# Kernel optimization log

Measured on AMD Instinct MI355X. Metric: run time of the kernel, lower is better.

## Reference

```python
import jax, jax.numpy as jnp
import numpy as np

B, T, F, C0, C1, H = 32, 1000, 32, 16, 8, 64
LSNR_SCALE, LSNR_OFFSET = 50.0, -15.0  # lsnr_max=35, lsnr_min=-15


def _conv1x3(x, w, b):
    # x: [N, Cin, T, F]; kernel (1,3), freq padding 1 (stride 1, k=1 so no time context)
    y = jax.lax.conv_general_dilated(x, w, (1, 1), [(0, 0), (1, 1)],
                                     dimension_numbers=('NCHW', 'OIHW', 'NCHW'))
    return y + b[None, :, None, None]


def _ln(x, g, b, eps=1e-5):
    # LayerNorm over the last (freq) axis, as nn.LayerNorm(n_freqs)
    mu = x.mean(-1, keepdims=True)
    var = x.var(-1, keepdims=True)
    return (x - mu) / jnp.sqrt(var + eps) * g + b


def _gru(x, wih, whh, bih, bhh):
    # PyTorch-style GRU. x: [S, N, D] -> (ys [S, N, Hh], h_last [N, Hh])
    Hh = whh.shape[1]
    h0 = jnp.zeros((x.shape[1], Hh), x.dtype)
    def step(h, xt):
        gi = xt @ wih.T + bih
        gh = h @ whh.T + bhh
        ir, iz, inn = jnp.split(gi, 3, axis=-1)
        hr, hz, hn = jnp.split(gh, 3, axis=-1)
        r = jax.nn.sigmoid(ir + hr)
        z = jax.nn.sigmoid(iz + hz)
        n = jnp.tanh(inn + r * hn)
        hnew = (1.0 - z) * n + z * h
        return hnew, hnew
    hT, ys = jax.lax.scan(step, h0, x)
    return ys, hT


def setup_inputs() -> dict:
    key = jax.random.key(0)
    ks = iter(jax.random.split(key, 40))
    def nrm(shape, s=0.02):
        return jax.random.normal(next(ks), shape, jnp.float32) * s
    return {
        'input': jax.random.normal(next(ks), (B, 1, T, F), jnp.float32),
        'conv0_w': nrm((C0, 1, 1, 3)), 'conv0_b': jnp.zeros((C0,), jnp.float32),
        'ln0_g': jnp.ones((F,), jnp.float32), 'ln0_b': jnp.zeros((F,), jnp.float32),
        'conv1_w': nrm((C1, C0, 1, 3)), 'conv1_b': jnp.zeros((C1,), jnp.float32),
        'ln1_g': jnp.ones((F,), jnp.float32), 'ln1_b': jnp.zeros((F,), jnp.float32),
        'q_w': nrm((H, C1, 1, 3)), 'q_b': jnp.zeros((H,), jnp.float32),
        'k_w': nrm((H, C1, 1, 3)), 'k_b': jnp.zeros((H,), jnp.float32),
        'v_w': nrm((H, C1, 1, 3)), 'v_b': jnp.zeros((H,), jnp.float32),
        'gruo_wih': nrm((3 * C1 * F, H * F)), 'gruo_whh': nrm((3 * C1 * F, C1 * F)),
        'gruo_bih': jnp.zeros((3 * C1 * F,), jnp.float32), 'gruo_bhh': jnp.zeros((3 * C1 * F,), jnp.float32),
        'ln_g': jnp.ones((F,), jnp.float32), 'ln_b': jnp.zeros((F,), jnp.float32),
        'grus_wih': nrm((48, C1 * F)), 'grus_whh': nrm((48, 16)),
        'grus_bih': jnp.zeros((48,), jnp.float32), 'grus_bhh': jnp.zeros((48,), jnp.float32),
        'fc_w': nrm((1, 16)), 'fc_b': jnp.zeros((1,), jnp.float32),
        'conv2_w': nrm((1, C1, 1, 3)), 'conv2_b': jnp.zeros((1,), jnp.float32),
        'ln2_g': jnp.ones((F,), jnp.float32), 'ln2_b': jnp.zeros((F,), jnp.float32),
    }


def reference(input, conv0_w, conv0_b, ln0_g, ln0_b, conv1_w, conv1_b, ln1_g, ln1_b,
              q_w, q_b, k_w, k_b, v_w, v_b, gruo_wih, gruo_whh, gruo_bih, gruo_bhh,
              ln_g, ln_b, grus_wih, grus_whh, grus_bih, grus_bhh, fc_w, fc_b,
              conv2_w, conv2_b, ln2_g, ln2_b):
    # conv0/conv1: conv -> LayerNorm(F) -> ReLU
    x0 = jax.nn.relu(_ln(_conv1x3(input, conv0_w, conv0_b), ln0_g, ln0_b))
    x1 = jax.nn.relu(_ln(_conv1x3(x0, conv1_w, conv1_b), ln1_g, ln1_b))  # [B,C1,T,F]
    # SpectalRecurrentAttention (no norm/act on q/k/v convs)
    q = _conv1x3(x1, q_w, q_b).transpose(0, 2, 3, 1)  # [B,T,F,H]
    k = _conv1x3(x1, k_w, k_b).transpose(0, 2, 1, 3)  # [B,T,H,F]
    v = _conv1x3(x1, v_w, v_b).transpose(0, 2, 3, 1)  # [B,T,F,H]
    w = jnp.einsum('btfh,bthg->btfg', q, k) / jnp.sqrt(jnp.float32(H))  # [B,T,F,F]
    # softmax2d: joint softmax over last two (freq x freq) dims
    w = jax.nn.softmax(w.reshape(B, T, F * F), axis=-1).reshape(B, T, F, F)
    att = jnp.einsum('btfg,btgh->btfh', w, v)  # [B,T,F,H]
    gi = att.reshape(B, T, F * H)
    ys, hT = _gru(gi.transpose(1, 0, 2), gruo_wih, gruo_whh, gruo_bih, gruo_bhh)  # over T (batch_first)
    o = ys.transpose(1, 0, 2)  # [B,T,C1*F]
    h_atten = hT[None]  # [1,B,C1*F]
    e = o.reshape(B, T, C1, F).transpose(0, 2, 1, 3)  # [B,C1,T,F]
    # gru_snr is NOT batch_first: it scans over dim0 (= B) of e.transpose(1,2).flatten(2,3) == o
    snr_ys, snr_hT = _gru(o, grus_wih, grus_whh, grus_bih, grus_bhh)  # ys [B,T,16], hT [T,16]
    h_snr = snr_hT[None]  # [1,T,16]
    lsnr = jax.nn.sigmoid(snr_ys @ fc_w.T + fc_b) * LSNR_SCALE + LSNR_OFFSET  # [B,T,1]
    xe = _ln(x1 + e, ln_g, ln_b)
    m = jax.nn.sigmoid(_ln(_conv1x3(xe, conv2_w, conv2_b), ln2_g, ln2_b))  # [B,1,T,F]
    return m, lsnr, h_atten, h_snr
```

## Files before the change

kernel.cpp:

```cpp
#include <hip/hip_runtime.h>


typedef unsigned short u16;
typedef u16 u16x8 __attribute__((ext_vector_type(8)));
typedef short s16x8 __attribute__((ext_vector_type(8)));
typedef float f32x4 __attribute__((ext_vector_type(4)));
typedef _Float16 h2t __attribute__((ext_vector_type(2)));
typedef unsigned int u32x16 __attribute__((ext_vector_type(16)));

__device__ __forceinline__ float sigf(float x) { return 1.f / (1.f + __expf(-x)); }
__device__ __forceinline__ float tanhfast(float x) { return 2.f / (1.f + __expf(-2.f * x)) - 1.f; }
__device__ __forceinline__ float bf2f(u16 s) { union { unsigned u; float f; } x; x.u = ((unsigned)s) << 16; return x.f; }
__device__ __forceinline__ u16 f2bf(float f) {
  union { float f; unsigned u; } x; x.f = f;
  unsigned r = x.u + 0x7fffu + ((x.u >> 16) & 1u);
  return (u16)(r >> 16);
}
__device__ __forceinline__ h2t pk(float a, float b) {
  auto v = __builtin_amdgcn_cvt_pkrtz(a, b);
  union { decltype(v) i; h2t o; } u; u.i = v; return u.o;
}
__device__ __forceinline__ h2t bch(unsigned x) { return __builtin_bit_cast(h2t, x); }

__global__ __launch_bounds__(256) void k_wcvt_all(
    const float* __restrict__ W, u16* __restrict__ Wb,
    const float* __restrict__ Wh, unsigned* __restrict__ Wp)
{
  if (blockIdx.x < 768) {
    const size_t i = ((size_t)blockIdx.x * 256 + threadIdx.x) * 8;
    float4 a = *(const float4*)(W + i);
    float4 b = *(const float4*)(W + i + 4);
    u16x8 o;
    o[0] = f2bf(a.x); o[1] = f2bf(a.y); o[2] = f2bf(a.z); o[3] = f2bf(a.w);
    o[4] = f2bf(b.x); o[5] = f2bf(b.y); o[6] = f2bf(b.z); o[7] = f2bf(b.w);
    *(u16x8*)(Wb + i) = o;
  } else {
    const size_t i = (size_t)(blockIdx.x - 768) * 256 + threadIdx.x;
    float2 a = *(const float2*)(Wh + i * 2);
    Wp[i] = __builtin_bit_cast(unsigned, pk(a.x, a.y));
  }
}

__global__ __launch_bounds__(256) void k_frontend(
    const float* __restrict__ in,
    const float* __restrict__ w0c, const float* __restrict__ b0c,
    const float* __restrict__ g0, const float* __restrict__ be0,
    const float* __restrict__ w1c, const float* __restrict__ b1c,
    const float* __restrict__ g1, const float* __restrict__ be1,
    const float* __restrict__ qw, const float* __restrict__ qb,
    const float* __restrict__ kw, const float* __restrict__ kb,
    const float* __restrict__ vw, const float* __restrict__ vb,
    int bt0, u16* __restrict__ x1g, u16* __restrict__ gi)
{
  const int bt = bt0 + blockIdx.x, tid = threadIdx.x;
  __shared__ float s_in[34];
  __shared__ float s_x0[16][34];
  __shared__ float s_x1[8][34];
  __shared__ float s_q[64][36];
  __shared__ float s_k[64][36];
  __shared__ float s_v[32][68];
  __shared__ float s_sc[32][36];
  __shared__ float s_red[8];
  __shared__ float s_mu[16], s_rs[16];

  if (tid < 32) s_in[1 + tid] = in[(size_t)bt * 32 + tid];
  if (tid == 0) { s_in[0] = 0.f; s_in[33] = 0.f; }
  __syncthreads();

  #pragma unroll
  for (int i = 0; i < 2; ++i) {
    int o = tid + i * 256, c = o >> 5, f = o & 31;
    float a = b0c[c] + w0c[c*3]*s_in[f] + w0c[c*3+1]*s_in[f+1] + w0c[c*3+2]*s_in[f+2];
    s_x0[c][1 + f] = a;
  }
  __syncthreads();
  {
    int c = tid >> 4, i = tid & 15;
    float a = s_x0[c][1 + i], b = s_x0[c][17 + i];
    float s = a + b, ss = a * a + b * b;
    #pragma unroll
    for (int m = 8; m >= 1; m >>= 1) { s += __shfl_xor(s, m); ss += __shfl_xor(ss, m); }
    if (i == 0) { float mu = s * (1.f/32.f); s_mu[c] = mu; s_rs[c] = rsqrtf(ss * (1.f/32.f) - mu*mu + 1e-5f); }
  }
  __syncthreads();
  #pragma unroll
  for (int i = 0; i < 2; ++i) {
    int o = tid + i * 256, c = o >> 5, f = o & 31;
    float v = (s_x0[c][1 + f] - s_mu[c]) * s_rs[c] * g0[f] + be0[f];
    s_x0[c][1 + f] = fmaxf(v, 0.f);
  }
  if (tid < 16) { s_x0[tid][0] = 0.f; s_x0[tid][33] = 0.f; }
  __syncthreads();

  {
    int c = tid >> 5, f = tid & 31;
    float a = b1c[c];
    #pragma unroll
    for (int cc = 0; cc < 16; ++cc) {
      const float* wr = w1c + (c * 16 + cc) * 3;
      a += wr[0]*s_x0[cc][f] + wr[1]*s_x0[cc][f+1] + wr[2]*s_x0[cc][f+2];
    }
    float s = a, ss = a * a;
    #pragma unroll
    for (int m = 16; m >= 1; m >>= 1) { s += __shfl_xor(s, m); ss += __shfl_xor(ss, m); }
    float mu = s * (1.f/32.f), rs = rsqrtf(ss * (1.f/32.f) - mu*mu + 1e-5f);
    float v = fmaxf((a - mu) * rs * g1[f] + be1[f], 0.f);
    s_x1[c][1 + f] = v;
    x1g[(size_t)bt * 256 + tid] = f2bf(v);
  }
  if (tid < 8) { s_x1[tid][0] = 0.f; s_x1[tid][33] = 0.f; }
  __syncthreads();

  {
    int h = tid >> 2, fg = tid & 3;
    float aq[8], ak[8], av[8];
    float qbv = qb[h], kbv = kb[h], vbv = vb[h];
    #pragma unroll
    for (int i = 0; i < 8; ++i) { aq[i] = qbv; ak[i] = kbv; av[i] = vbv; }
    #pragma unroll
    for (int c = 0; c < 8; ++c) {
      const float* qr = qw + (h * 8 + c) * 3;
      const float* kr = kw + (h * 8 + c) * 3;
      const float* vr = vw + (h * 8 + c) * 3;
      float q0 = qr[0], q1 = qr[1], q2 = qr[2];
      float k0 = kr[0], k1 = kr[1], k2 = kr[2];
      float v0 = vr[0], v1 = vr[1], v2 = vr[2];
      #pragma unroll
      for (int i = 0; i < 8; ++i) {
        int f = fg + i * 4;
        float xa = s_x1[c][f], xb = s_x1[c][f+1], xc = s_x1[c][f+2];
        aq[i] += q0*xa + q1*xb + q2*xc;
        ak[i] += k0*xa + k1*xb + k2*xc;
        av[i] += v0*xa + v1*xb + v2*xc;
      }
    }
    #pragma unroll
    for (int i = 0; i < 8; ++i) {
      int f = fg + i * 4;
      s_q[h][f] = aq[i];
      s_k[h][f] = ak[i];
      s_v[f][h] = av[i];
    }
  }
  __syncthreads();

  const int sf = tid >> 3, sgq = tid & 7;
  float sc0 = 0.f, sc1 = 0.f, sc2 = 0.f, sc3 = 0.f;
  #pragma unroll 8
  for (int h = 0; h < 64; ++h) {
    float q = s_q[h][sf];
    float4 k4 = *(const float4*)&s_k[h][sgq * 4];
    sc0 += q * k4.x; sc1 += q * k4.y; sc2 += q * k4.z; sc3 += q * k4.w;
  }
  sc0 *= 0.125f; sc1 *= 0.125f; sc2 *= 0.125f; sc3 *= 0.125f;
  float mx = fmaxf(fmaxf(sc0, sc1), fmaxf(sc2, sc3));
  #pragma unroll
  for (int m = 32; m >= 1; m >>= 1) mx = fmaxf(mx, __shfl_xor(mx, m));
  if ((tid & 63) == 0) s_red[tid >> 6] = mx;
  __syncthreads();
  mx = fmaxf(fmaxf(s_red[0], s_red[1]), fmaxf(s_red[2], s_red[3]));
  sc0 = __expf(sc0 - mx); sc1 = __expf(sc1 - mx);
  sc2 = __expf(sc2 - mx); sc3 = __expf(sc3 - mx);
  float sm = sc0 + sc1 + sc2 + sc3;
  #pragma unroll
  for (int m = 32; m >= 1; m >>= 1) sm += __shfl_xor(sm, m);
  __syncthreads();
  if ((tid & 63) == 0) s_red[4 + (tid >> 6)] = sm;
  __syncthreads();
  float inv = 1.f / (s_red[4] + s_red[5] + s_red[6] + s_red[7]);
  {
    float4 o4; o4.x = sc0 * inv; o4.y = sc1 * inv; o4.z = sc2 * inv; o4.w = sc3 * inv;
    *(float4*)&s_sc[sf][sgq * 4] = o4;
  }
  __syncthreads();

  {
    const int f = tid >> 3, hq = tid & 7;
    float a0=0,a1=0,a2=0,a3=0,a4=0,a5=0,a6=0,a7=0;
    #pragma unroll 8
    for (int g = 0; g < 32; ++g) {
      float w = s_sc[f][g];
      float4 v0 = *(const float4*)&s_v[g][hq * 8];
      float4 v1 = *(const float4*)&s_v[g][hq * 8 + 4];
      a0 += w * v0.x; a1 += w * v0.y; a2 += w * v0.z; a3 += w * v0.w;
      a4 += w * v1.x; a5 += w * v1.y; a6 += w * v1.z; a7 += w * v1.w;
    }
    u16x8 ov;
    ov[0] = f2bf(a0); ov[1] = f2bf(a1); ov[2] = f2bf(a2); ov[3] = f2bf(a3);
    ov[4] = f2bf(a4); ov[5] = f2bf(a5); ov[6] = f2bf(a6); ov[7] = f2bf(a7);
    *(u16x8*)(gi + (size_t)blockIdx.x * 2048 + f * 64 + hq * 8) = ov;
  }
}

__global__ __launch_bounds__(512, 2) void k_gemm_mfma(
    const u16* __restrict__ A, const u16* __restrict__ Wb,
    const float* __restrict__ bias, u16* __restrict__ C, int M)
{
  __shared__ u16 lA[128][40];
  __shared__ u16 lB[256][40];
  const int tid = threadIdx.x;
  const int m0 = blockIdx.x * 128, n0 = blockIdx.y * 256;
  const int w = tid >> 6, l = tid & 63;
  const int wr = w >> 2, wc = w & 3;
  const int fr = l & 15, fg = l >> 4;
  f32x4 acc[4][4] = {};
  const int ar = tid >> 2, akc = tid & 3;
  const int br = tid >> 1, bkc = tid & 1;
  for (int k0 = 0; k0 < 2048; k0 += 32) {
    int am = m0 + ar;
    u16x8 av = (u16x8)(u16)0;
    if (am < M) av = *(const u16x8*)(A + (size_t)am * 2048 + k0 + akc * 8);
    *(u16x8*)&lA[ar][akc * 8] = av;
    const u16* bp = Wb + (size_t)(n0 + br) * 2048 + k0 + bkc * 16;
    u16x8 bv0 = *(const u16x8*)bp;
    u16x8 bv1 = *(const u16x8*)(bp + 8);
    *(u16x8*)&lB[br][bkc * 16] = bv0;
    *(u16x8*)&lB[br][bkc * 16 + 8] = bv1;
    __syncthreads();
    #pragma unroll
    for (int mi = 0; mi < 4; ++mi) {
      s16x8 afr = *(const s16x8*)&lA[wr * 64 + mi * 16 + fr][fg * 8];
      #pragma unroll
      for (int ni = 0; ni < 4; ++ni) {
        s16x8 bfr = *(const s16x8*)&lB[wc * 64 + ni * 16 + fr][fg * 8];
        acc[mi][ni] = __builtin_amdgcn_mfma_f32_16x16x32_bf16(afr, bfr, acc[mi][ni], 0, 0, 0);
      }
    }
    __syncthreads();
  }
  #pragma unroll
  for (int mi = 0; mi < 4; ++mi) {
    #pragma unroll
    for (int ni = 0; ni < 4; ++ni) {
      int col = n0 + wc * 64 + ni * 16 + (l & 15);
      float bv = bias[col];
      #pragma unroll
      for (int i = 0; i < 4; ++i) {
        int row = m0 + wr * 64 + mi * 16 + (l >> 4) * 4 + i;
        if (row < M) C[(size_t)row * 768 + col] = f2bf(acc[mi][ni][i] + bv);
      }
    }
  }
}

#define LD16(V, P, Q) { \
  uint4 a_ = (P)[(Q)*4+0], b_ = (P)[(Q)*4+1], c_ = (P)[(Q)*4+2], d_ = (P)[(Q)*4+3]; \
  V[0]=a_.x; V[1]=a_.y; V[2]=a_.z; V[3]=a_.w; \
  V[4]=b_.x; V[5]=b_.y; V[6]=b_.z; V[7]=b_.w; \
  V[8]=c_.x; V[9]=c_.y; V[10]=c_.z; V[11]=c_.w; \
  V[12]=d_.x; V[13]=d_.y; V[14]=d_.z; V[15]=d_.w; }

#define D1(H, W, E, acc) acc = __builtin_amdgcn_fdot2((H), bch((W)[E]), (acc), false);
#define BLK(C, WR, WZ, WN, E) { \
  uint4 hv_ = hp[C]; \
  h2t h0_ = bch(hv_.x), h1_ = bch(hv_.y), h2_ = bch(hv_.z), h3_ = bch(hv_.w); \
  D1(h0_, WR, (E)+0, pr0) D1(h0_, WZ, (E)+0, pz0) D1(h0_, WN, (E)+0, pn0) \
  D1(h1_, WR, (E)+1, pr1) D1(h1_, WZ, (E)+1, pz1) D1(h1_, WN, (E)+1, pn1) \
  D1(h2_, WR, (E)+2, pr0) D1(h2_, WZ, (E)+2, pz0) D1(h2_, WN, (E)+2, pn0) \
  D1(h3_, WR, (E)+3, pr1) D1(h3_, WZ, (E)+3, pz1) D1(h3_, WN, (E)+3, pn1) }

__global__ __launch_bounds__(512) void k_gru_batch(
    const u16* __restrict__ gih, const unsigned* __restrict__ wpk,
    const float* __restrict__ bhh, u16* __restrict__ ob,
    float* __restrict__ hatt, int b0)
{
  __shared__ h2t s_h2[2][136];
  const int tid = threadIdx.x;
  const int u = tid >> 1, part = tid & 1;
  const int bl = blockIdx.x;
  const int b = b0 + bl;

  const uint4* wr4 = (const uint4*)(wpk + ((size_t)(      u) * 128) + part * 64);
  const uint4* wz4 = (const uint4*)(wpk + ((size_t)(256 + u) * 128) + part * 64);
  const uint4* wn4 = (const uint4*)(wpk + ((size_t)(512 + u) * 128) + part * 64);

  u32x16 wr0, wr1, wr2, wr3, wz0, wz1, wz2, wz3, wn0, wn1, wn2, wn3;
  LD16(wr0, wr4, 0) LD16(wr1, wr4, 1) LD16(wr2, wr4, 2) LD16(wr3, wr4, 3)
  LD16(wz0, wz4, 0) LD16(wz1, wz4, 1) LD16(wz2, wz4, 2) LD16(wz3, wz4, 3)
  LD16(wn0, wn4, 0) LD16(wn1, wn4, 1) LD16(wn2, wn4, 2) LD16(wn3, wn4, 3)

  float bh_r = 0.f, bh_z = 0.f, bh_n = 0.f;
  if (part == 0) { bh_r = bhh[u]; bh_z = bhh[256 + u]; bh_n = bhh[512 + u]; }
  if (tid < 128) s_h2[0][tid + (tid >> 6) * 4] = pk(0.f, 0.f);
  __syncthreads();

  float hprev = 0.f;
  int cur = 0;
  for (int t = 0; t < 1000; ++t) {
    float gi_r = 0.f, gi_z = 0.f, gi_n = 0.f;
    if (part == 0) {
      const u16* gr_ = gih + ((size_t)bl * 1000 + t) * 768;
      gi_r = bf2f(gr_[u]); gi_z = bf2f(gr_[256 + u]); gi_n = bf2f(gr_[512 + u]);
    }
    const uint4* hp = (const uint4*)&s_h2[cur][part * 68];
    float pr0 = 0.f, pr1 = 0.f, pz0 = 0.f, pz1 = 0.f, pn0 = 0.f, pn1 = 0.f;
    BLK( 0, wr0, wz0, wn0,  0) BLK( 1, wr0, wz0, wn0,  4)
    BLK( 2, wr0, wz0, wn0,  8) BLK( 3, wr0, wz0, wn0, 12)
    BLK( 4, wr1, wz1, wn1,  0) BLK( 5, wr1, wz1, wn1,  4)
    BLK( 6, wr1, wz1, wn1,  8) BLK( 7, wr1, wz1, wn1, 12)
    BLK( 8, wr2, wz2, wn2,  0) BLK( 9, wr2, wz2, wn2,  4)
    BLK(10, wr2, wz2, wn2,  8) BLK(11, wr2, wz2, wn2, 12)
    BLK(12, wr3, wz3, wn3,  0) BLK(13, wr3, wz3, wn3,  4)
    BLK(14, wr3, wz3, wn3,  8) BLK(15, wr3, wz3, wn3, 12)
    float pr = pr0 + pr1, pz = pz0 + pz1, pn = pn0 + pn1;
    pr += __shfl_xor(pr, 1);
    pz += __shfl_xor(pz, 1);
    pn += __shfl_xor(pn, 1);
    float hnew = 0.f;
    if (part == 0) {
      float r = sigf(gi_r + pr + bh_r);
      float z = sigf(gi_z + pz + bh_z);
      float n = tanhfast(gi_n + r * (pn + bh_n));
      hnew = (1.f - z) * n + z * hprev;
      hprev = hnew;
      ob[((size_t)b * 1000 + t) * 256 + u] = f2bf(hnew);
    }
    float hother = __shfl_xor(hnew, 2);
    if ((tid & 3) == 0) {
      int j = tid >> 2;
      s_h2[cur ^ 1][j + (j >> 6) * 4] = pk(hnew, hother);
    }
    asm volatile("s_waitcnt lgkmcnt(0)" ::: "memory");
    __builtin_amdgcn_s_barrier();
    cur ^= 1;
  }
  if (part == 0) hatt[b * 256 + u] = hprev;
}

__global__ __launch_bounds__(256) void k_gru_snr(
    const u16* __restrict__ ob, const float* __restrict__ wih,
    const float* __restrict__ whh, const float* __restrict__ bih,
    const float* __restrict__ bhh, const float* __restrict__ fcw,
    const float* __restrict__ fcb,
    float* __restrict__ lsnr_out, float* __restrict__ hsnr_out)
{
  __shared__ float s_wi[48][260];
  __shared__ float s_wh[48][20];
  __shared__ float s_o[16][260];
  __shared__ float s_h[16][20];
  const int tid = threadIdx.x, wg = blockIdx.x;
  const int n0 = wg * 16;
  for (int i = tid; i < 48 * 256; i += 256) s_wi[i >> 8][i & 255] = wih[i];
  for (int i = tid; i < 768; i += 256) s_wh[i >> 4][i & 15] = whh[i];
  const int n = tid >> 4, u = tid & 15;
  const bool valid = (n0 + n) < 1000;
  s_h[n][u] = 0.f;
  float hcur = 0.f;
  const float bi_r = bih[u], bi_z = bih[16 + u], bi_n = bih[32 + u];
  const float bh_r = bhh[u], bh_z = bhh[16 + u], bh_n = bhh[32 + u];
  const float fw = fcw[u], fb = fcb[0];
  __syncthreads();
  for (int step = 0; step < 32; ++step) {
    for (int i = tid; i < 512; i += 256) {
      int nn = i >> 5, c8 = (i & 31) * 8;
      int row = n0 + nn;
      if (row < 1000) {
        u16x8 v = *(const u16x8*)(ob + ((size_t)step * 1000 + row) * 256 + c8);
        #pragma unroll
        for (int j = 0; j < 8; ++j) s_o[nn][c8 + j] = bf2f(v[j]);
      } else {
        #pragma unroll
        for (int j = 0; j < 8; ++j) s_o[nn][c8 + j] = 0.f;
      }
    }
    __syncthreads();
    float gr = bi_r, gz = bi_z, gn = bi_n;
    {
      const float4* o4 = (const float4*)&s_o[n][0];
      const float4* wr = (const float4*)&s_wi[u][0];
      const float4* wz = (const float4*)&s_wi[16 + u][0];
      const float4* wn = (const float4*)&s_wi[32 + u][0];
      #pragma unroll 4
      for (int k4 = 0; k4 < 64; ++k4) {
        float4 ov = o4[k4];
        float4 a = wr[k4], c = wz[k4], d = wn[k4];
        gr += ov.x*a.x + ov.y*a.y + ov.z*a.z + ov.w*a.w;
        gz += ov.x*c.x + ov.y*c.y + ov.z*c.z + ov.w*c.w;
        gn += ov.x*d.x + ov.y*d.y + ov.z*d.z + ov.w*d.w;
      }
    }
    float hr = bh_r, hz = bh_z, hn_ = bh_n;
    #pragma unroll
    for (int k = 0; k < 16; ++k) {
      float hv = s_h[n][k];
      hr  += s_wh[u][k] * hv;
      hz  += s_wh[16 + u][k] * hv;
      hn_ += s_wh[32 + u][k] * hv;
    }
    float r = sigf(gr + hr);
    float z = sigf(gz + hz);
    float nn2 = tanhfast(gn + r * hn_);
    float hnew = (1.f - z) * nn2 + z * hcur;
    __syncthreads();
    s_h[n][u] = hnew;
    hcur = hnew;
    float part = hnew * fw;
    #pragma unroll
    for (int m = 8; m >= 1; m >>= 1) part += __shfl_xor(part, m);
    if (u == 0 && valid) lsnr_out[step * 1000 + n0 + n] = sigf(part + fb) * 50.f - 15.f;
    __syncthreads();
  }
  if (valid) hsnr_out[(size_t)(n0 + n) * 16 + u] = hcur;
}

__global__ __launch_bounds__(256) void k_final(
    const u16* __restrict__ x1g, const u16* __restrict__ ob,
    const float* __restrict__ lng, const float* __restrict__ lnb,
    const float* __restrict__ c2w, const float* __restrict__ c2b,
    const float* __restrict__ g2, const float* __restrict__ be2,
    float* __restrict__ m_out)
{
  const int bt = blockIdx.x, tid = threadIdx.x;
  __shared__ float s_xe[8][34];
  __shared__ float s_y[32];
  const int c = tid >> 5, f = tid & 31;
  float v = bf2f(x1g[(size_t)bt * 256 + tid]) + bf2f(ob[(size_t)bt * 256 + tid]);
  float s = v, ss = v * v;
  #pragma unroll
  for (int m = 16; m >= 1; m >>= 1) { s += __shfl_xor(s, m); ss += __shfl_xor(ss, m); }
  float mu = s * (1.f/32.f), rs = rsqrtf(ss * (1.f/32.f) - mu * mu + 1e-5f);
  s_xe[c][1 + f] = (v - mu) * rs * lng[f] + lnb[f];
  if (tid < 8) { s_xe[tid][0] = 0.f; s_xe[tid][33] = 0.f; }
  __syncthreads();
  if (tid < 32) {
    float a = c2b[0];
    #pragma unroll
    for (int cc = 0; cc < 8; ++cc) {
      const float* wr = c2w + cc * 3;
      a += wr[0]*s_xe[cc][tid] + wr[1]*s_xe[cc][tid+1] + wr[2]*s_xe[cc][tid+2];
    }
    s_y[tid] = a;
  }
  __syncthreads();
  if (tid < 32) {
    float y = s_y[tid];
    float s2 = y, ss2 = y * y;
    #pragma unroll
    for (int m = 16; m >= 1; m >>= 1) { s2 += __shfl_xor(s2, m); ss2 += __shfl_xor(ss2, m); }
    float mu2 = s2 * (1.f/32.f), rs2 = rsqrtf(ss2 * (1.f/32.f) - mu2 * mu2 + 1e-5f);
    float yn = (y - mu2) * rs2 * g2[tid] + be2[tid];
    m_out[(size_t)bt * 32 + tid] = sigf(yn);
  }
}

extern "C" void kernel_launch(void* const* d_in, const int* in_sizes, int n_in,
                              void* d_out, int out_size, void* d_ws, size_t ws_size,
                              hipStream_t stream)
{
  const float* input = (const float*)d_in[0];
  const float* w0    = (const float*)d_in[1];
  const float* b0    = (const float*)d_in[2];
  const float* ln0g  = (const float*)d_in[3];
  const float* ln0b  = (const float*)d_in[4];
  const float* w1    = (const float*)d_in[5];
  const float* b1    = (const float*)d_in[6];
  const float* ln1g  = (const float*)d_in[7];
  const float* ln1b  = (const float*)d_in[8];
  const float* qw    = (const float*)d_in[9];
  const float* qb    = (const float*)d_in[10];
  const float* kw    = (const float*)d_in[11];
  const float* kb    = (const float*)d_in[12];
  const float* vw    = (const float*)d_in[13];
  const float* vb    = (const float*)d_in[14];
  const float* gwih  = (const float*)d_in[15];
  const float* gwhh  = (const float*)d_in[16];
  const float* gbih  = (const float*)d_in[17];
  const float* gbhh  = (const float*)d_in[18];
  const float* lng   = (const float*)d_in[19];
  const float* lnb   = (const float*)d_in[20];
  const float* swih  = (const float*)d_in[21];
  const float* swhh  = (const float*)d_in[22];
  const float* sbih  = (const float*)d_in[23];
  const float* sbhh  = (const float*)d_in[24];
  const float* fcw   = (const float*)d_in[25];
  const float* fcb   = (const float*)d_in[26];
  const float* c2w   = (const float*)d_in[27];
  const float* c2b   = (const float*)d_in[28];
  const float* ln2g  = (const float*)d_in[29];
  const float* ln2b  = (const float*)d_in[30];
  (void)in_sizes; (void)n_in; (void)out_size;

  char* ws = (char*)d_ws;
  size_t off = 0;
  auto take = [&](size_t bytes) -> void* {
    void* p = ws + off;
    off += (bytes + 255) & ~(size_t)255;
    return p;
  };
  u16* x1g      = (u16*)take((size_t)32000 * 256 * 2);
  u16* ob       = (u16*)take((size_t)32000 * 256 * 2);
  u16* gwb      = (u16*)take((size_t)768 * 2048 * 2);
  unsigned* wpk = (unsigned*)take((size_t)768 * 128 * 4);

  const size_t fixedoff = off;
  int GB = 32;
  while (GB > 1) {
    size_t need = fixedoff + ((size_t)GB * 1000 * 768 * 2 + 256)
                           + ((size_t)4096 * 2048 * 2 + 256);
    if (need <= ws_size) break;
    GB >>= 1;
  }
  u16* gih = (u16*)take((size_t)GB * 1000 * 768 * 2);
  int CH = GB * 1000;
  while (CH > 4096) {
    if (off + ((size_t)CH * 2048 * 2 + 256) <= ws_size) break;
    CH >>= 1;
  }
  if (CH > GB * 1000) CH = GB * 1000;
  CH = (CH + 63) & ~63;
  u16* gi = (u16*)take((size_t)CH * 2048 * 2);

  float* out      = (float*)d_out;
  float* m_out    = out;
  float* lsnr_out = out + 1024000;
  float* hatt_out = out + 1056000;
  float* hsnr_out = out + 1064192;

  k_wcvt_all<<<1152, 256, 0, stream>>>(gwih, gwb, gwhh, wpk);

  const int NG = 32 / GB;
  for (int g = 0; g < NG; ++g) {
    const int row0 = g * GB * 1000, rows = GB * 1000;
    for (int c0 = 0; c0 < rows; c0 += CH) {
      const int Mc = (rows - c0 < CH) ? (rows - c0) : CH;
      k_frontend<<<Mc, 256, 0, stream>>>(input, w0, b0, ln0g, ln0b, w1, b1,
                                         ln1g, ln1b, qw, qb, kw, kb, vw, vb,
                                         row0 + c0, x1g, gi);
      dim3 gg((Mc + 127) / 128, 3);
      k_gemm_mfma<<<gg, 512, 0, stream>>>(gi, gwb, gbih, gih + (size_t)c0 * 768, Mc);
    }
    k_gru_batch<<<GB, 512, 0, stream>>>(gih, wpk, gbhh, ob, hatt_out, g * GB);
  }
  k_gru_snr<<<64, 256, 0, stream>>>(ob, swih, swhh, sbih, sbhh, fcw, fcb,
                                    lsnr_out, hsnr_out);
  k_final<<<32000, 256, 0, stream>>>(x1g, ob, lng, lnb, c2w, c2b, ln2g, ln2b, m_out);
}
```

Before: 2.230 ms.

## Split each batch GRU recurrence across two workgroups with global-memory hidden-state exchange

Each batch element's 256-unit GRU recurrence now runs on two workgroups, each owning 128 hidden units. This halves the per-thread weight registers and the dot-product work per step. After every timestep the two halves swap their new hidden state through a double-buffered global array and spin on a release/acquire flag, then merge it into shared memory. The cost is an inter-CU handshake with global atomics and extra barriers on every one of the 1000 sequential steps. Both halves must also be resident at once, or the kernel deadlocks.

```diff
diff --git a/kernel.cpp b/kernel.cpp
--- a/kernel.cpp
+++ b/kernel.cpp
@@ -21,10 +21,12 @@
   union { decltype(v) i; h2t o; } u; u.i = v; return u.o;
 }
 __device__ __forceinline__ h2t bch(unsigned x) { return __builtin_bit_cast(h2t, x); }
+__device__ __forceinline__ unsigned bcu(h2t x) { return __builtin_bit_cast(unsigned, x); }
 
 __global__ __launch_bounds__(256) void k_wcvt_all(
     const float* __restrict__ W, u16* __restrict__ Wb,
-    const float* __restrict__ Wh, unsigned* __restrict__ Wp)
+    const float* __restrict__ Wh, unsigned* __restrict__ Wp,
+    int* __restrict__ hflag)
 {
   if (blockIdx.x < 768) {
     const size_t i = ((size_t)blockIdx.x * 256 + threadIdx.x) * 8;
@@ -34,10 +36,14 @@
     o[0] = f2bf(a.x); o[1] = f2bf(a.y); o[2] = f2bf(a.z); o[3] = f2bf(a.w);
     o[4] = f2bf(b.x); o[5] = f2bf(b.y); o[6] = f2bf(b.z); o[7] = f2bf(b.w);
     *(u16x8*)(Wb + i) = o;
-  } else {
+  } else if (blockIdx.x < 1152) {
     const size_t i = (size_t)(blockIdx.x - 768) * 256 + threadIdx.x;
     float2 a = *(const float2*)(Wh + i * 2);
     Wp[i] = __builtin_bit_cast(unsigned, pk(a.x, a.y));
+  } else {
+    if (threadIdx.x < 64)
+      __hip_atomic_store(&hflag[threadIdx.x], 0, __ATOMIC_RELAXED,
+                         __HIP_MEMORY_SCOPE_AGENT);
   }
 }
 
@@ -259,30 +265,40 @@
   D1(h2_, WR, (E)+2, pr0) D1(h2_, WZ, (E)+2, pz0) D1(h2_, WN, (E)+2, pn0) \
   D1(h3_, WR, (E)+3, pr1) D1(h3_, WZ, (E)+3, pz1) D1(h3_, WN, (E)+3, pn1) }
 
+__device__ __forceinline__ int hslot(int j) { return j + (j >> 5) * 4; }
+
 __global__ __launch_bounds__(512) void k_gru_batch(
     const u16* __restrict__ gih, const unsigned* __restrict__ wpk,
     const float* __restrict__ bhh, u16* __restrict__ ob,
-    float* __restrict__ hatt, int b0)
-{
-  __shared__ h2t s_h2[2][136];
+    float* __restrict__ hatt, unsigned* __restrict__ hx,
+    int* __restrict__ hflag, int b0)
+{
+  __shared__ h2t s_h2[2][140];
   const int tid = threadIdx.x;
-  const int u = tid >> 1, part = tid & 1;
-  const int bl = blockIdx.x;
+  const int bl = blockIdx.x >> 1;
+  const int half = blockIdx.x & 1;
   const int b = b0 + bl;
-
-  const uint4* wr4 = (const uint4*)(wpk + ((size_t)(      u) * 128) + part * 64);
-  const uint4* wz4 = (const uint4*)(wpk + ((size_t)(256 + u) * 128) + part * 64);
-  const uint4* wn4 = (const uint4*)(wpk + ((size_t)(512 + u) * 128) + part * 64);
-
-  u32x16 wr0, wr1, wr2, wr3, wz0, wz1, wz2, wz3, wn0, wn1, wn2, wn3;
-  LD16(wr0, wr4, 0) LD16(wr1, wr4, 1) LD16(wr2, wr4, 2) LD16(wr3, wr4, 3)
-  LD16(wz0, wz4, 0) LD16(wz1, wz4, 1) LD16(wz2, wz4, 2) LD16(wz3, wz4, 3)
-  LD16(wn0, wn4, 0) LD16(wn1, wn4, 1) LD16(wn2, wn4, 2) LD16(wn3, wn4, 3)
+  const int u_local = tid >> 2, part = tid & 3;
+  const int u = half * 128 + u_local;
+
+  const uint4* wr4 = (const uint4*)(wpk + ((size_t)(      u) * 128) + part * 32);
+  const uint4* wz4 = (const uint4*)(wpk + ((size_t)(256 + u) * 128) + part * 32);
+  const uint4* wn4 = (const uint4*)(wpk + ((size_t)(512 + u) * 128) + part * 32);
+
+  u32x16 wrA, wrB, wzA, wzB, wnA, wnB;
+  LD16(wrA, wr4, 0) LD16(wrB, wr4, 1)
+  LD16(wzA, wz4, 0) LD16(wzB, wz4, 1)
+  LD16(wnA, wn4, 0) LD16(wnB, wn4, 1)
 
   float bh_r = 0.f, bh_z = 0.f, bh_n = 0.f;
   if (part == 0) { bh_r = bhh[u]; bh_z = bhh[256 + u]; bh_n = bhh[512 + u]; }
-  if (tid < 128) s_h2[0][tid + (tid >> 6) * 4] = pk(0.f, 0.f);
-  __syncthreads();
+  if (tid < 128) s_h2[0][hslot(tid)] = pk(0.f, 0.f);
+  __syncthreads();
+
+  unsigned* hx_own = hx + ((size_t)b * 2 + half) * 64;
+  unsigned* hx_par = hx + ((size_t)b * 2 + (half ^ 1)) * 64;
+  int* flag_own = hflag + b * 2 + half;
+  int* flag_par = hflag + b * 2 + (half ^ 1);
 
   float hprev = 0.f;
   int cur = 0;
@@ -292,20 +308,16 @@
       const u16* gr_ = gih + ((size_t)bl * 1000 + t) * 768;
       gi_r = bf2f(gr_[u]); gi_z = bf2f(gr_[256 + u]); gi_n = bf2f(gr_[512 + u]);
     }
-    const uint4* hp = (const uint4*)&s_h2[cur][part * 68];
+    const uint4* hp = (const uint4*)&s_h2[cur][part * 36];
     float pr0 = 0.f, pr1 = 0.f, pz0 = 0.f, pz1 = 0.f, pn0 = 0.f, pn1 = 0.f;
-    BLK( 0, wr0, wz0, wn0,  0) BLK( 1, wr0, wz0, wn0,  4)
-    BLK( 2, wr0, wz0, wn0,  8) BLK( 3, wr0, wz0, wn0, 12)
-    BLK( 4, wr1, wz1, wn1,  0) BLK( 5, wr1, wz1, wn1,  4)
-    BLK( 6, wr1, wz1, wn1,  8) BLK( 7, wr1, wz1, wn1, 12)
-    BLK( 8, wr2, wz2, wn2,  0) BLK( 9, wr2, wz2, wn2,  4)
-    BLK(10, wr2, wz2, wn2,  8) BLK(11, wr2, wz2, wn2, 12)
-    BLK(12, wr3, wz3, wn3,  0) BLK(13, wr3, wz3, wn3,  4)
-    BLK(14, wr3, wz3, wn3,  8) BLK(15, wr3, wz3, wn3, 12)
+    BLK(0, wrA, wzA, wnA,  0) BLK(1, wrA, wzA, wnA,  4)
+    BLK(2, wrA, wzA, wnA,  8) BLK(3, wrA, wzA, wnA, 12)
+    BLK(4, wrB, wzB, wnB,  0) BLK(5, wrB, wzB, wnB,  4)
+    BLK(6, wrB, wzB, wnB,  8) BLK(7, wrB, wzB, wnB, 12)
     float pr = pr0 + pr1, pz = pz0 + pz1, pn = pn0 + pn1;
-    pr += __shfl_xor(pr, 1);
-    pz += __shfl_xor(pz, 1);
-    pn += __shfl_xor(pn, 1);
+    pr += __shfl_xor(pr, 1); pr += __shfl_xor(pr, 2);
+    pz += __shfl_xor(pz, 1); pz += __shfl_xor(pz, 2);
+    pn += __shfl_xor(pn, 1); pn += __shfl_xor(pn, 2);
     float hnew = 0.f;
     if (part == 0) {
       float r = sigf(gi_r + pr + bh_r);
@@ -315,10 +327,30 @@
       hprev = hnew;
       ob[((size_t)b * 1000 + t) * 256 + u] = f2bf(hnew);
     }
-    float hother = __shfl_xor(hnew, 2);
-    if ((tid & 3) == 0) {
-      int j = tid >> 2;
-      s_h2[cur ^ 1][j + (j >> 6) * 4] = pk(hnew, hother);
+    float hother = __shfl_xor(hnew, 4);
+    const size_t pofs = (size_t)(t & 1) * 4096;
+    if ((tid & 7) == 0) {
+      int j = tid >> 3;
+      h2t pv = pk(hnew, hother);
+      int jg = half * 64 + j;
+      s_h2[cur ^ 1][hslot(jg)] = pv;
+      __hip_atomic_store(&hx_own[pofs + j], bcu(pv), __ATOMIC_RELAXED,
+                         __HIP_MEMORY_SCOPE_AGENT);
+    }
+    __syncthreads();
+    if (tid == 0) {
+      __hip_atomic_store(flag_own, t + 1, __ATOMIC_RELEASE,
+                         __HIP_MEMORY_SCOPE_AGENT);
+      while (__hip_atomic_load(flag_par, __ATOMIC_ACQUIRE,
+                               __HIP_MEMORY_SCOPE_AGENT) < t + 1)
+        __builtin_amdgcn_s_sleep(1);
+    }
+    __syncthreads();
+    if (tid < 64) {
+      unsigned v = __hip_atomic_load(&hx_par[pofs + tid], __ATOMIC_RELAXED,
+                                     __HIP_MEMORY_SCOPE_AGENT);
+      int jg = (half ^ 1) * 64 + tid;
+      s_h2[cur ^ 1][hslot(jg)] = bch(v);
     }
     asm volatile("s_waitcnt lgkmcnt(0)" ::: "memory");
     __builtin_amdgcn_s_barrier();
@@ -491,6 +523,8 @@
   u16* ob       = (u16*)take((size_t)32000 * 256 * 2);
   u16* gwb      = (u16*)take((size_t)768 * 2048 * 2);
   unsigned* wpk = (unsigned*)take((size_t)768 * 128 * 4);
+  unsigned* hx  = (unsigned*)take((size_t)2 * 32 * 2 * 64 * 4);
+  int* hflag    = (int*)take((size_t)64 * 4);
 
   const size_t fixedoff = off;
   int GB = 32;
@@ -516,7 +550,7 @@
   float* hatt_out = out + 1056000;
   float* hsnr_out = out + 1064192;
 
-  k_wcvt_all<<<1152, 256, 0, stream>>>(gwih, gwb, gwhh, wpk);
+  k_wcvt_all<<<1153, 256, 0, stream>>>(gwih, gwb, gwhh, wpk, hflag);
 
   const int NG = 32 / GB;
   for (int g = 0; g < NG; ++g) {
@@ -529,7 +563,8 @@
       dim3 gg((Mc + 127) / 128, 3);
       k_gemm_mfma<<<gg, 512, 0, stream>>>(gi, gwb, gbih, gih + (size_t)c0 * 768, Mc);
     }
-    k_gru_batch<<<GB, 512, 0, stream>>>(gih, wpk, gbhh, ob, hatt_out, g * GB);
+    k_gru_batch<<<2 * GB, 512, 0, stream>>>(gih, wpk, gbhh, ob, hatt_out,
+                                            hx, hflag, g * GB);
   }
   k_gru_snr<<<64, 256, 0, stream>>>(ob, swih, swhh, sbih, sbhh, fcw, fcb,
                                     lsnr_out, hsnr_out);
```

New measurement: 4.119 ms. 1.85x slower.
